# Optimization experiments

Hardware: AMD Instinct MI355X
Metric: run time of the kernel (lower is better)

Reference implementation:

```python
import jax, jax.numpy as jnp
import numpy as np

RADIUS = 2.0  # ball-query radius (float forward arg in the original; fixed here)


def _conv1x1(x, W, b):
    # 1x1 Conv2D over NHWC == per-point linear layer
    return jnp.einsum('bmsc,cd->bmsd', x, W) + b


def _ball_query(xyz, new_xyz, radius, nsample):
    """For each cluster center, take the first (by index) nsample points within
    radius, padding with the first found neighbor (TF ball-query semantics).
    xyz: (B,N,3), new_xyz: (B,M,3) -> idx (B,M,nsample) int32."""
    N = xyz.shape[1]
    d2 = jnp.sum((new_xyz[:, :, None, :] - xyz[:, None, :, :]) ** 2, axis=-1)  # (B,M,N)
    valid = d2 < radius * radius
    key = jnp.where(valid, jnp.arange(N, dtype=jnp.int32)[None, None, :], N)
    order = jnp.argsort(key, axis=-1)[..., :nsample]          # (B,M,nsample)
    skey = jnp.take_along_axis(key, order, axis=-1)
    idx = jnp.where(skey < N, order, order[..., :1])          # pad with first neighbor
    return idx


def setup_inputs() -> dict:
    key = jax.random.key(0)
    ks = jax.random.split(key, 8)
    B, N = 8, 8192
    xyz = jax.random.normal(ks[0], (B, N, 3), dtype=jnp.float32)

    def w(k, cin, cout):
        return (jax.random.normal(k, (cin, cout), dtype=jnp.float32) / np.sqrt(cin)).astype(jnp.float32)

    z = lambda c: jnp.zeros((c,), jnp.float32)
    inp = {
        'xyz': xyz,
        'W1': w(ks[1], 3, 64),    'b1': z(64),
        'W2': w(ks[2], 64, 128),  'b2': z(128),
        'W3': w(ks[3], 128, 256), 'b3': z(256),
        'W4': w(ks[4], 256, 128), 'b4': z(128),
        'W5': w(ks[5], 128, 64),  'b5': z(64),
        'Wa': w(ks[6], 64, 1),    'ba': z(1),
        'Wo': w(ks[7], 64, 2),    'bo': z(2),
        'num_clusters': 512,
        'num_samples': 64,
    }
    return inp


def reference(xyz, W1, b1, W2, b2, W3, b3, W4, b4, W5, b5, Wa, ba, Wo, bo,
              num_clusters, num_samples):
    # sample cluster centers (deterministic stand-in for random subsampling)
    new_xyz = xyz[:, :num_clusters]                                    # (B,M,3)
    idx = _ball_query(xyz, new_xyz, RADIUS, num_samples)               # (B,M,S)
    grouped = jax.vmap(lambda pts, i: pts[i])(xyz, idx)                # (B,M,S,3)
    g = (grouped - new_xyz[:, :, None, :]) / RADIUS                    # normalize_radius

    # shared per-point MLP (1x1 convs, relu)
    h = jax.nn.relu(_conv1x1(g, W1, b1))
    h = jax.nn.relu(_conv1x1(h, W2, b2))
    h = jax.nn.relu(_conv1x1(h, W3, b3))
    # MaxPoolAxis: max over samples, keepdims
    h = jnp.max(h, axis=2, keepdims=True)                              # (B,M,1,256)
    # mlp2 convs (linear, no activation in source)
    h = _conv1x1(h, W4, b4)
    h = _conv1x1(h, W5, b5)                                            # (B,M,1,64)

    attention = jax.nn.softplus(_conv1x1(h, Wa, ba))[:, :, 0, 0]       # (B,M)
    o = _conv1x1(h, Wo, bo)[:, :, 0, :]                                # (B,M,2)
    o = o / jnp.sqrt(jnp.maximum(jnp.sum(o * o, axis=-1, keepdims=True), 1e-8))
    orientation = jnp.arctan2(o[..., 1], o[..., 0])                    # (B,M)
    return new_xyz, idx, attention, orientation
```

## Files before the change

kernel.cpp:

```cpp
#include <hip/hip_runtime.h>
#include <math.h>

#define BB 8
#define NN 8192
#define MM 512
#define SS 64
#define NCLUST (BB*MM)

#define OUT_IDX   (BB*MM*3)
#define OUT_ATT   (OUT_IDX + BB*MM*SS)
#define OUT_ORI   (OUT_ATT + BB*MM)

#define WS_W3 8192
#define WS_V  40960

typedef short v8s __attribute__((ext_vector_type(8)));
typedef float v4f __attribute__((ext_vector_type(4)));

static __device__ __forceinline__ unsigned short f2bf(float x) {
    unsigned int u = __float_as_uint(x);
    u += 0x7FFFu + ((u >> 16) & 1u);
    return (unsigned short)(u >> 16);
}

__global__ void pack_weights(const float* __restrict__ W2,
                             const float* __restrict__ W3,
                             unsigned short* __restrict__ ws)
{
    const int gid = blockIdx.x * 256 + threadIdx.x;
    const float* W; unsigned short* dst; int N, kt, nt, lane;
    if (gid < 1024) {
        W = W2; N = 128;
        const int tile = gid >> 6; lane = gid & 63;
        kt = tile >> 3; nt = tile & 7;
        dst = ws + (size_t)(tile * 64 + lane) * 8;
    } else {
        const int g = gid - 1024;
        W = W3; N = 256;
        const int tile = g >> 6; lane = g & 63;
        kt = tile >> 4; nt = tile & 15;
        dst = ws + WS_W3 + (size_t)(tile * 64 + lane) * 8;
    }
    const int k0 = kt * 32 + (lane >> 4) * 8;
    const int n  = nt * 16 + (lane & 15);
    union { unsigned short u[8]; v8s v; } f;
    #pragma unroll
    for (int j = 0; j < 8; ++j) f.u[j] = f2bf(W[(k0 + j) * N + n]);
    *(v8s*)dst = f.v;
}

__global__ __launch_bounds__(256, 4) void feat3d_front(
    const float* __restrict__ xyz,
    const float* __restrict__ W1, const float* __restrict__ b1,
    const float* __restrict__ b2, const float* __restrict__ b3,
    const unsigned short* __restrict__ Wp,
    unsigned short* __restrict__ vdst,
    float* __restrict__ out)
{
    __shared__ __align__(16) unsigned char lds[27200];
    unsigned short* a2p = (unsigned short*)lds;
    unsigned short* a3p = (unsigned short*)(lds + 8192);
    float* smallf       = (float*)(lds + 24576);
    int* ls_idx         = (int*)(lds + 26624);
    unsigned long long* ls_mask = (unsigned long long*)(lds + 26880);

    float* ls_g  = smallf;
    float* ls_w1 = smallf + 256;

    const int t   = threadIdx.x;
    const int wv  = t >> 6;
    const int l   = t & 63;
    const int q   = l >> 4;
    const int r16 = l & 15;
    const int blk = blockIdx.x;
    const int b   = blk >> 9;
    const int m   = blk & 511;
    const float* xb = xyz + (size_t)b * (NN * 3);

    const v8s* W2f = (const v8s*)Wp;
    v8s bfr[2][2];
    #pragma unroll
    for (int kt = 0; kt < 2; ++kt)
        #pragma unroll
        for (int ni = 0; ni < 2; ++ni)
            bfr[kt][ni] = W2f[(kt*8 + 2*wv + ni)*64 + l];

    const float cx = xb[m*3+0], cy = xb[m*3+1], cz = xb[m*3+2];

    if (t < 3) out[(b*MM + m)*3 + t] = xb[m*3 + t];

    if (t < 64) {
        ls_w1[t*4+0] = W1[t];
        ls_w1[t*4+1] = W1[64 + t];
        ls_w1[t*4+2] = W1[128 + t];
        ls_w1[t*4+3] = b1[t];
    }

    int cnt = 0;
    {
        int base = 0, pb = 0;
        while (base < NN && cnt < SS) {
            const int j = base + t;
            const float dx = xb[j*3+0] - cx;
            const float dy = xb[j*3+1] - cy;
            const float dz = xb[j*3+2] - cz;
            const float d2 = __fadd_rn(__fadd_rn(__fmul_rn(dx,dx), __fmul_rn(dy,dy)),
                                       __fmul_rn(dz,dz));
            const bool valid = d2 < 4.0f;
            const unsigned long long mask = __ballot(valid);
            if (l == 0) ls_mask[pb*4 + wv] = mask;
            __syncthreads();
            const unsigned long long m0 = ls_mask[pb*4+0], m1 = ls_mask[pb*4+1],
                                     m2 = ls_mask[pb*4+2], m3 = ls_mask[pb*4+3];
            int below = __popcll(mask & ((1ull << l) - 1ull));
            if (wv > 0) below += (int)__popcll(m0);
            if (wv > 1) below += (int)__popcll(m1);
            if (wv > 2) below += (int)__popcll(m2);
            const int pos = cnt + below;
            if (valid && pos < SS) {
                ls_idx[pos]   = j;
                ls_g[pos*4+0] = dx * 0.5f;
                ls_g[pos*4+1] = dy * 0.5f;
                ls_g[pos*4+2] = dz * 0.5f;
            }
            cnt += (int)(__popcll(m0) + __popcll(m1) + __popcll(m2) + __popcll(m3));
            if (cnt > SS) cnt = SS;
            base += 256;
            pb ^= 1;
        }
    }
    __syncthreads();
    if (t < SS && t >= cnt) {
        ls_idx[t]   = ls_idx[0];
        ls_g[t*4+0] = ls_g[0];
        ls_g[t*4+1] = ls_g[1];
        ls_g[t*4+2] = ls_g[2];
    }
    __syncthreads();
    if (t < 64) out[OUT_IDX + (b*MM + m)*SS + t] = (float)ls_idx[t];

    {
        const int s = wv*16 + r16;
        const float4 g4 = *(const float4*)&ls_g[s*4];
        #pragma unroll
        for (int kt = 0; kt < 2; ++kt) {
            union { unsigned short u[8]; v8s v; } fr;
            #pragma unroll
            for (int j = 0; j < 8; ++j) {
                const int c = kt*32 + q*8 + j;
                const float4 w = *(const float4*)&ls_w1[c*4];
                const float h = fmaf(g4.x, w.x, fmaf(g4.y, w.y, fmaf(g4.z, w.z, w.w)));
                fr.u[j] = f2bf(fmaxf(h, 0.f));
            }
            *(v8s*)&a2p[((kt*4 + wv)*64 + l)*8] = fr.v;
        }
    }
    __syncthreads();

    {
        const v4f z = {0.f, 0.f, 0.f, 0.f};
        v4f acc[4][2];
        #pragma unroll
        for (int mt = 0; mt < 4; ++mt) { acc[mt][0] = z; acc[mt][1] = z; }

        #pragma unroll
        for (int kt = 0; kt < 2; ++kt)
            #pragma unroll
            for (int mt = 0; mt < 4; ++mt) {
                const v8s a = *(const v8s*)&a2p[((kt*4 + mt)*64 + l)*8];
                #pragma unroll
                for (int ni = 0; ni < 2; ++ni)
                    acc[mt][ni] = __builtin_amdgcn_mfma_f32_16x16x32_bf16(
                        a, bfr[kt][ni], acc[mt][ni], 0, 0, 0);
            }

        #pragma unroll
        for (int ni = 0; ni < 2; ++ni) {
            const int c2  = (2*wv + ni)*16 + r16;
            const float bias = b2[c2];
            const int kt3 = c2 >> 5;
            const int lhi = ((c2 >> 3) & 3) << 4;
            const int j3  = c2 & 7;
            #pragma unroll
            for (int mt = 0; mt < 4; ++mt)
                #pragma unroll
                for (int rg = 0; rg < 4; ++rg) {
                    const float h = fmaxf(acc[mt][ni][rg] + bias, 0.f);
                    const int s15 = q*4 + rg;
                    a3p[((kt3*4 + mt)*64 + (lhi | s15))*8 + j3] = f2bf(h);
                }
        }
    }
    __syncthreads();

    {
        const v8s* W3f = (const v8s*)(Wp + WS_W3);
        const int cg = blk;
        unsigned short* vrow = vdst + (size_t)cg * 256;

        #pragma unroll
        for (int np = 0; np < 2; ++np) {
            const int nt0 = 4*wv + 2*np;
            const v4f z = {0.f, 0.f, 0.f, 0.f};
            v4f acc[4][2];
            #pragma unroll
            for (int mt = 0; mt < 4; ++mt) { acc[mt][0] = z; acc[mt][1] = z; }

            v8s bb0 = W3f[(0*16 + nt0    )*64 + l];
            v8s bb1 = W3f[(0*16 + nt0 + 1)*64 + l];
            #pragma unroll
            for (int kt = 0; kt < 4; ++kt) {
                v8s a[4];
                #pragma unroll
                for (int mt = 0; mt < 4; ++mt)
                    a[mt] = *(const v8s*)&a3p[((kt*4 + mt)*64 + l)*8];
                v8s nb0, nb1;
                if (kt < 3) {
                    nb0 = W3f[((kt+1)*16 + nt0    )*64 + l];
                    nb1 = W3f[((kt+1)*16 + nt0 + 1)*64 + l];
                }
                #pragma unroll
                for (int mt = 0; mt < 4; ++mt) {
                    acc[mt][0] = __builtin_amdgcn_mfma_f32_16x16x32_bf16(
                        a[mt], bb0, acc[mt][0], 0, 0, 0);
                    acc[mt][1] = __builtin_amdgcn_mfma_f32_16x16x32_bf16(
                        a[mt], bb1, acc[mt][1], 0, 0, 0);
                }
                if (kt < 3) { bb0 = nb0; bb1 = nb1; }
            }

            #pragma unroll
            for (int ni = 0; ni < 2; ++ni) {
                float mx = acc[0][ni][0];
                #pragma unroll
                for (int mt = 0; mt < 4; ++mt)
                    #pragma unroll
                    for (int rg = 0; rg < 4; ++rg)
                        mx = fmaxf(mx, acc[mt][ni][rg]);
                mx = fmaxf(mx, __shfl_xor(mx, 16));
                mx = fmaxf(mx, __shfl_xor(mx, 32));
                if (q == 0) {
                    const int c = (nt0 + ni)*16 + r16;
                    vrow[c] = f2bf(fmaxf(mx + b3[c], 0.f));
                }
            }
        }
    }
}

__global__ __launch_bounds__(256) void feat3d_tail(
    const unsigned short* __restrict__ vsrc,
    const float* __restrict__ W4, const float* __restrict__ b4,
    const float* __restrict__ W5, const float* __restrict__ b5,
    const float* __restrict__ Wa, const float* __restrict__ ba,
    const float* __restrict__ Wo, const float* __restrict__ bo,
    float* __restrict__ out)
{
    __shared__ __align__(16) float V[16][256];
    __shared__ __align__(16) float H4[16][128];
    __shared__ __align__(16) float H5[16][64];

    const int t   = threadIdx.x;
    const int cl0 = blockIdx.x * 16;

    {
        const int i  = t >> 4;
        const int ch = t & 15;
        const uint4* src = (const uint4*)(vsrc + (size_t)(cl0 + i) * 256);
        #pragma unroll
        for (int h = 0; h < 2; ++h) {
            const uint4 r = src[ch*2 + h];
            const unsigned int u[4] = {r.x, r.y, r.z, r.w};
            #pragma unroll
            for (int j = 0; j < 4; ++j) {
                V[i][ch*16 + h*8 + 2*j]     = __uint_as_float(u[j] << 16);
                V[i][ch*16 + h*8 + 2*j + 1] = __uint_as_float(u[j] & 0xFFFF0000u);
            }
        }
    }
    __syncthreads();

    {
        const int c  = t & 127;
        const int ih = t >> 7;
        float acc[8];
        #pragma unroll
        for (int i = 0; i < 8; ++i) acc[i] = b4[c];
        for (int k4 = 0; k4 < 64; ++k4) {
            const float w0 = W4[(4*k4+0)*128 + c];
            const float w1 = W4[(4*k4+1)*128 + c];
            const float w2 = W4[(4*k4+2)*128 + c];
            const float w3 = W4[(4*k4+3)*128 + c];
            #pragma unroll
            for (int i = 0; i < 8; ++i) {
                const float4 vv = *(const float4*)&V[ih*8 + i][4*k4];
                acc[i] = fmaf(vv.x, w0, fmaf(vv.y, w1,
                         fmaf(vv.z, w2, fmaf(vv.w, w3, acc[i]))));
            }
        }
        #pragma unroll
        for (int i = 0; i < 8; ++i) H4[ih*8 + i][c] = acc[i];
    }
    __syncthreads();

    {
        const int c  = t & 63;
        const int iq = t >> 6;
        float acc[4];
        #pragma unroll
        for (int i = 0; i < 4; ++i) acc[i] = b5[c];
        for (int k4 = 0; k4 < 32; ++k4) {
            const float w0 = W5[(4*k4+0)*64 + c];
            const float w1 = W5[(4*k4+1)*64 + c];
            const float w2 = W5[(4*k4+2)*64 + c];
            const float w3 = W5[(4*k4+3)*64 + c];
            #pragma unroll
            for (int i = 0; i < 4; ++i) {
                const float4 vv = *(const float4*)&H4[iq*4 + i][4*k4];
                acc[i] = fmaf(vv.x, w0, fmaf(vv.y, w1,
                         fmaf(vv.z, w2, fmaf(vv.w, w3, acc[i]))));
            }
        }
        #pragma unroll
        for (int i = 0; i < 4; ++i) H5[iq*4 + i][c] = acc[i];
    }
    __syncthreads();

    {
        const int wv = t >> 6, l = t & 63;
        const float wa  = Wa[l];
        const float wo0 = Wo[2*l + 0];
        const float wo1 = Wo[2*l + 1];
        #pragma unroll
        for (int i = 0; i < 4; ++i) {
            const float hv = H5[4*wv + i][l];
            float va = hv * wa;
            float v0 = hv * wo0;
            float v1 = hv * wo1;
            #pragma unroll
            for (int off = 32; off > 0; off >>= 1) {
                va += __shfl_down(va, off);
                v0 += __shfl_down(v0, off);
                v1 += __shfl_down(v1, off);
            }
            if (l == 0) {
                const int cg = cl0 + 4*wv + i;
                const float a = va + ba[0];
                out[OUT_ATT + cg] = fmaxf(a, 0.f) + log1pf(expf(-fabsf(a)));
                out[OUT_ORI + cg] = atan2f(v1 + bo[1], v0 + bo[0]);
            }
        }
    }
}

extern "C" void kernel_launch(void* const* d_in, const int* in_sizes, int n_in,
                              void* d_out, int out_size, void* d_ws, size_t ws_size,
                              hipStream_t stream) {
    const float* xyz = (const float*)d_in[0];
    const float* W1  = (const float*)d_in[1];
    const float* b1  = (const float*)d_in[2];
    const float* W2  = (const float*)d_in[3];
    const float* b2  = (const float*)d_in[4];
    const float* W3  = (const float*)d_in[5];
    const float* b3  = (const float*)d_in[6];
    const float* W4  = (const float*)d_in[7];
    const float* b4  = (const float*)d_in[8];
    const float* W5  = (const float*)d_in[9];
    const float* b5  = (const float*)d_in[10];
    const float* Wa  = (const float*)d_in[11];
    const float* ba  = (const float*)d_in[12];
    const float* Wo  = (const float*)d_in[13];
    const float* bo  = (const float*)d_in[14];

    unsigned short* ws = (unsigned short*)d_ws;

    pack_weights<<<dim3(20), dim3(256), 0, stream>>>(W2, W3, ws);
    feat3d_front<<<dim3(NCLUST), dim3(256), 0, stream>>>(
        xyz, W1, b1, b2, b3, ws, ws + WS_V, (float*)d_out);
    feat3d_tail<<<dim3(NCLUST/16), dim3(256), 0, stream>>>(
        ws + WS_V, W4, b4, W5, b5, Wa, ba, Wo, bo, (float*)d_out);
}
```

Baseline: 139.0 us.

## Process two clusters per block with per-wave ball query and shared MLP tiles

Each block now handles two cluster centers, with waves 0 and 1 each doing an independent wave-local ball query using ballot prefix counts, removing the block-wide barrier in every scan iteration. The MLP MFMA stages are widened to 128 rows so W2/W3 fragments loaded per wave are reused across both clusters, halving weight traffic per cluster and the block count. In exchange, LDS use grows, register pressure rises (occupancy bound lowered to 3), half the waves idle during the query, and each query scans only 64 points per step.

```diff
diff --git a/kernel.cpp b/kernel.cpp
--- a/kernel.cpp
+++ b/kernel.cpp
@@ -49,7 +49,7 @@
     *(v8s*)dst = f.v;
 }
 
-__global__ __launch_bounds__(256, 4) void feat3d_front(
+__global__ __launch_bounds__(256, 3) void feat3d_front(
     const float* __restrict__ xyz,
     const float* __restrict__ W1, const float* __restrict__ b1,
     const float* __restrict__ b2, const float* __restrict__ b3,
@@ -57,24 +57,20 @@
     unsigned short* __restrict__ vdst,
     float* __restrict__ out)
 {
-    __shared__ __align__(16) unsigned char lds[27200];
+    __shared__ __align__(16) unsigned char lds[52736];
     unsigned short* a2p = (unsigned short*)lds;
-    unsigned short* a3p = (unsigned short*)(lds + 8192);
-    float* smallf       = (float*)(lds + 24576);
-    int* ls_idx         = (int*)(lds + 26624);
-    unsigned long long* ls_mask = (unsigned long long*)(lds + 26880);
-
-    float* ls_g  = smallf;
-    float* ls_w1 = smallf + 256;
+    unsigned short* a3p = (unsigned short*)(lds + 16384);
+    float* ls_g  = (float*)(lds + 49152);
+    float* ls_w1 = (float*)(lds + 51200);
+    int*   ls_idx= (int*)(lds + 52224);
 
     const int t   = threadIdx.x;
     const int wv  = t >> 6;
     const int l   = t & 63;
     const int q   = l >> 4;
     const int r16 = l & 15;
-    const int blk = blockIdx.x;
-    const int b   = blk >> 9;
-    const int m   = blk & 511;
+    const int cg0 = blockIdx.x * 2;
+    const int b   = cg0 >> 9;
     const float* xb = xyz + (size_t)b * (NN * 3);
 
     const v8s* W2f = (const v8s*)Wp;
@@ -85,22 +81,24 @@
         for (int ni = 0; ni < 2; ++ni)
             bfr[kt][ni] = W2f[(kt*8 + 2*wv + ni)*64 + l];
 
-    const float cx = xb[m*3+0], cy = xb[m*3+1], cz = xb[m*3+2];
-
-    if (t < 3) out[(b*MM + m)*3 + t] = xb[m*3 + t];
-
-    if (t < 64) {
-        ls_w1[t*4+0] = W1[t];
-        ls_w1[t*4+1] = W1[64 + t];
-        ls_w1[t*4+2] = W1[128 + t];
-        ls_w1[t*4+3] = b1[t];
-    }
-
-    int cnt = 0;
-    {
-        int base = 0, pb = 0;
+    if (t >= 128 && t < 192) {
+        const int tt = t - 128;
+        ls_w1[tt*4+0] = W1[tt];
+        ls_w1[tt*4+1] = W1[64 + tt];
+        ls_w1[tt*4+2] = W1[128 + tt];
+        ls_w1[tt*4+3] = b1[tt];
+    }
+
+    if (wv < 2) {
+        const int cg = cg0 + wv;
+        const int m  = cg & 511;
+        const float cx = xb[m*3+0], cy = xb[m*3+1], cz = xb[m*3+2];
+        if (l < 3) out[cg*3 + l] = xb[m*3 + l];
+        float* gdst = ls_g  + wv * 256;
+        int*   idst = ls_idx + wv * 64;
+        int cnt = 0, base = 0;
         while (base < NN && cnt < SS) {
-            const int j = base + t;
+            const int j = base + l;
             const float dx = xb[j*3+0] - cx;
             const float dy = xb[j*3+1] - cy;
             const float dz = xb[j*3+2] - cz;
@@ -108,70 +106,66 @@
                                        __fmul_rn(dz,dz));
             const bool valid = d2 < 4.0f;
             const unsigned long long mask = __ballot(valid);
-            if (l == 0) ls_mask[pb*4 + wv] = mask;
-            __syncthreads();
-            const unsigned long long m0 = ls_mask[pb*4+0], m1 = ls_mask[pb*4+1],
-                                     m2 = ls_mask[pb*4+2], m3 = ls_mask[pb*4+3];
-            int below = __popcll(mask & ((1ull << l) - 1ull));
-            if (wv > 0) below += (int)__popcll(m0);
-            if (wv > 1) below += (int)__popcll(m1);
-            if (wv > 2) below += (int)__popcll(m2);
+            const int below = __popcll(mask & ((1ull << l) - 1ull));
             const int pos = cnt + below;
             if (valid && pos < SS) {
-                ls_idx[pos]   = j;
-                ls_g[pos*4+0] = dx * 0.5f;
-                ls_g[pos*4+1] = dy * 0.5f;
-                ls_g[pos*4+2] = dz * 0.5f;
-            }
-            cnt += (int)(__popcll(m0) + __popcll(m1) + __popcll(m2) + __popcll(m3));
+                idst[pos]   = j;
+                gdst[pos*4+0] = dx * 0.5f;
+                gdst[pos*4+1] = dy * 0.5f;
+                gdst[pos*4+2] = dz * 0.5f;
+            }
+            cnt += (int)__popcll(mask);
             if (cnt > SS) cnt = SS;
-            base += 256;
-            pb ^= 1;
-        }
-    }
-    __syncthreads();
-    if (t < SS && t >= cnt) {
-        ls_idx[t]   = ls_idx[0];
-        ls_g[t*4+0] = ls_g[0];
-        ls_g[t*4+1] = ls_g[1];
-        ls_g[t*4+2] = ls_g[2];
-    }
-    __syncthreads();
-    if (t < 64) out[OUT_IDX + (b*MM + m)*SS + t] = (float)ls_idx[t];
-
-    {
-        const int s = wv*16 + r16;
-        const float4 g4 = *(const float4*)&ls_g[s*4];
-        #pragma unroll
-        for (int kt = 0; kt < 2; ++kt) {
-            union { unsigned short u[8]; v8s v; } fr;
-            #pragma unroll
-            for (int j = 0; j < 8; ++j) {
-                const int c = kt*32 + q*8 + j;
-                const float4 w = *(const float4*)&ls_w1[c*4];
-                const float h = fmaf(g4.x, w.x, fmaf(g4.y, w.y, fmaf(g4.z, w.z, w.w)));
-                fr.u[j] = f2bf(fmaxf(h, 0.f));
-            }
-            *(v8s*)&a2p[((kt*4 + wv)*64 + l)*8] = fr.v;
+            base += 64;
+        }
+        if (l >= cnt) {
+            idst[l]     = idst[0];
+            gdst[l*4+0] = gdst[0];
+            gdst[l*4+1] = gdst[1];
+            gdst[l*4+2] = gdst[2];
+        }
+        out[OUT_IDX + cg*SS + l] = (float)idst[l];
+    }
+    __syncthreads();
+
+    {
+        #pragma unroll
+        for (int cc = 0; cc < 2; ++cc) {
+            const int rr = cc*64 + wv*16 + r16;
+            const int mt = rr >> 4;
+            const float4 g4 = *(const float4*)&ls_g[rr*4];
+            #pragma unroll
+            for (int kt = 0; kt < 2; ++kt) {
+                union { unsigned short u[8]; v8s v; } fr;
+                #pragma unroll
+                for (int j = 0; j < 8; ++j) {
+                    const int c = kt*32 + q*8 + j;
+                    const float4 w = *(const float4*)&ls_w1[c*4];
+                    const float h = fmaf(g4.x, w.x, fmaf(g4.y, w.y,
+                                    fmaf(g4.z, w.z, w.w)));
+                    fr.u[j] = f2bf(fmaxf(h, 0.f));
+                }
+                *(v8s*)&a2p[((kt*8 + mt)*64 + l)*8] = fr.v;
+            }
         }
     }
     __syncthreads();
 
     {
         const v4f z = {0.f, 0.f, 0.f, 0.f};
-        v4f acc[4][2];
-        #pragma unroll
-        for (int mt = 0; mt < 4; ++mt) { acc[mt][0] = z; acc[mt][1] = z; }
+        v4f acc[8][2];
+        #pragma unroll
+        for (int mt = 0; mt < 8; ++mt) { acc[mt][0] = z; acc[mt][1] = z; }
 
         #pragma unroll
         for (int kt = 0; kt < 2; ++kt)
             #pragma unroll
-            for (int mt = 0; mt < 4; ++mt) {
-                const v8s a = *(const v8s*)&a2p[((kt*4 + mt)*64 + l)*8];
-                #pragma unroll
-                for (int ni = 0; ni < 2; ++ni)
-                    acc[mt][ni] = __builtin_amdgcn_mfma_f32_16x16x32_bf16(
-                        a, bfr[kt][ni], acc[mt][ni], 0, 0, 0);
+            for (int mt = 0; mt < 8; ++mt) {
+                const v8s a = *(const v8s*)&a2p[((kt*8 + mt)*64 + l)*8];
+                acc[mt][0] = __builtin_amdgcn_mfma_f32_16x16x32_bf16(
+                    a, bfr[kt][0], acc[mt][0], 0, 0, 0);
+                acc[mt][1] = __builtin_amdgcn_mfma_f32_16x16x32_bf16(
+                    a, bfr[kt][1], acc[mt][1], 0, 0, 0);
             }
 
         #pragma unroll
@@ -182,12 +176,12 @@
             const int lhi = ((c2 >> 3) & 3) << 4;
             const int j3  = c2 & 7;
             #pragma unroll
-            for (int mt = 0; mt < 4; ++mt)
+            for (int mt = 0; mt < 8; ++mt)
                 #pragma unroll
                 for (int rg = 0; rg < 4; ++rg) {
                     const float h = fmaxf(acc[mt][ni][rg] + bias, 0.f);
                     const int s15 = q*4 + rg;
-                    a3p[((kt3*4 + mt)*64 + (lhi | s15))*8 + j3] = f2bf(h);
+                    a3p[((kt3*8 + mt)*64 + (lhi | s15))*8 + j3] = f2bf(h);
                 }
         }
     }
@@ -195,32 +189,32 @@
 
     {
         const v8s* W3f = (const v8s*)(Wp + WS_W3);
-        const int cg = blk;
-        unsigned short* vrow = vdst + (size_t)cg * 256;
+        unsigned short* vrow0 = vdst + (size_t)cg0 * 256;
+        unsigned short* vrow1 = vdst + (size_t)(cg0 + 1) * 256;
 
         #pragma unroll
         for (int np = 0; np < 2; ++np) {
             const int nt0 = 4*wv + 2*np;
             const v4f z = {0.f, 0.f, 0.f, 0.f};
-            v4f acc[4][2];
-            #pragma unroll
-            for (int mt = 0; mt < 4; ++mt) { acc[mt][0] = z; acc[mt][1] = z; }
-
-            v8s bb0 = W3f[(0*16 + nt0    )*64 + l];
-            v8s bb1 = W3f[(0*16 + nt0 + 1)*64 + l];
+            v4f acc[8][2];
+            #pragma unroll
+            for (int mt = 0; mt < 8; ++mt) { acc[mt][0] = z; acc[mt][1] = z; }
+
+            v8s bb0 = W3f[(nt0    )*64 + l];
+            v8s bb1 = W3f[(nt0 + 1)*64 + l];
             #pragma unroll
             for (int kt = 0; kt < 4; ++kt) {
-                v8s a[4];
-                #pragma unroll
-                for (int mt = 0; mt < 4; ++mt)
-                    a[mt] = *(const v8s*)&a3p[((kt*4 + mt)*64 + l)*8];
+                v8s a[8];
+                #pragma unroll
+                for (int mt = 0; mt < 8; ++mt)
+                    a[mt] = *(const v8s*)&a3p[((kt*8 + mt)*64 + l)*8];
                 v8s nb0, nb1;
                 if (kt < 3) {
                     nb0 = W3f[((kt+1)*16 + nt0    )*64 + l];
                     nb1 = W3f[((kt+1)*16 + nt0 + 1)*64 + l];
                 }
                 #pragma unroll
-                for (int mt = 0; mt < 4; ++mt) {
+                for (int mt = 0; mt < 8; ++mt) {
                     acc[mt][0] = __builtin_amdgcn_mfma_f32_16x16x32_bf16(
                         a[mt], bb0, acc[mt][0], 0, 0, 0);
                     acc[mt][1] = __builtin_amdgcn_mfma_f32_16x16x32_bf16(
@@ -231,17 +225,23 @@
 
             #pragma unroll
             for (int ni = 0; ni < 2; ++ni) {
-                float mx = acc[0][ni][0];
+                float mx0 = acc[0][ni][0], mx1 = acc[4][ni][0];
                 #pragma unroll
                 for (int mt = 0; mt < 4; ++mt)
                     #pragma unroll
-                    for (int rg = 0; rg < 4; ++rg)
-                        mx = fmaxf(mx, acc[mt][ni][rg]);
-                mx = fmaxf(mx, __shfl_xor(mx, 16));
-                mx = fmaxf(mx, __shfl_xor(mx, 32));
+                    for (int rg = 0; rg < 4; ++rg) {
+                        mx0 = fmaxf(mx0, acc[mt    ][ni][rg]);
+                        mx1 = fmaxf(mx1, acc[mt + 4][ni][rg]);
+                    }
+                mx0 = fmaxf(mx0, __shfl_xor(mx0, 16));
+                mx0 = fmaxf(mx0, __shfl_xor(mx0, 32));
+                mx1 = fmaxf(mx1, __shfl_xor(mx1, 16));
+                mx1 = fmaxf(mx1, __shfl_xor(mx1, 32));
                 if (q == 0) {
                     const int c = (nt0 + ni)*16 + r16;
-                    vrow[c] = f2bf(fmaxf(mx + b3[c], 0.f));
+                    const float bc = b3[c];
+                    vrow0[c] = f2bf(fmaxf(mx0 + bc, 0.f));
+                    vrow1[c] = f2bf(fmaxf(mx1 + bc, 0.f));
                 }
             }
         }
@@ -375,7 +375,7 @@
     unsigned short* ws = (unsigned short*)d_ws;
 
     pack_weights<<<dim3(20), dim3(256), 0, stream>>>(W2, W3, ws);
-    feat3d_front<<<dim3(NCLUST), dim3(256), 0, stream>>>(
+    feat3d_front<<<dim3(NCLUST/2), dim3(256), 0, stream>>>(
         xyz, W1, b1, b2, b3, ws, ws + WS_V, (float*)d_out);
     feat3d_tail<<<dim3(NCLUST/16), dim3(256), 0, stream>>>(
         ws + WS_V, W4, b4, W5, b5, Wa, ba, Wo, bo, (float*)d_out);
```

Result: slower. 156.0 us (+12.3%).

## Split ball query into its own wave-per-cluster kernel before the MLP kernel

Applied to the files above, without the earlier changes.

Moves the ball query out of the fused front kernel into a separate kernel where each 64-lane wave handles one cluster, so the scan needs only a wave ballot instead of block-wide LDS mask exchange and __syncthreads every iteration. Grouped offsets go to a global workspace that the MLP kernel then reads, which now has smaller LDS and a higher occupancy hint. In exchange it adds a kernel launch and a global round trip for the grouped coordinates, and each wave scans 64 points per step instead of 256 per block.

```diff
diff --git a/kernel.cpp b/kernel.cpp
--- a/kernel.cpp
+++ b/kernel.cpp
@@ -13,6 +13,7 @@
 
 #define WS_W3 8192
 #define WS_V  40960
+#define WS_G  1089536
 
 typedef short v8s __attribute__((ext_vector_type(8)));
 typedef float v4f __attribute__((ext_vector_type(4)));
@@ -49,23 +50,67 @@
     *(v8s*)dst = f.v;
 }
 
-__global__ __launch_bounds__(256, 4) void feat3d_front(
+__global__ __launch_bounds__(256, 8) void feat3d_bq(
     const float* __restrict__ xyz,
+    float* __restrict__ gws,
+    float* __restrict__ out)
+{
+    const int t  = threadIdx.x;
+    const int l  = t & 63;
+    const int cg = blockIdx.x * 4 + (t >> 6);
+    const int b  = cg >> 9;
+    const int m  = cg & 511;
+    const float* xb = xyz + (size_t)b * (NN * 3);
+
+    const float cx = xb[m*3+0], cy = xb[m*3+1], cz = xb[m*3+2];
+    if (l < 3) out[cg*3 + l] = xb[m*3 + l];
+
+    float4* gdst = (float4*)(gws + (size_t)cg * 256);
+    float*  idst = out + OUT_IDX + (size_t)cg * SS;
+
+    int cnt = 0, base = 0, fIdx = -1;
+    float fx = 0.f, fy = 0.f, fz = 0.f;
+    while (base < NN && cnt < SS) {
+        const int j = base + l;
+        const float dx = xb[j*3+0] - cx;
+        const float dy = xb[j*3+1] - cy;
+        const float dz = xb[j*3+2] - cz;
+        const float d2 = __fadd_rn(__fadd_rn(__fmul_rn(dx,dx), __fmul_rn(dy,dy)),
+                                   __fmul_rn(dz,dz));
+        const bool valid = d2 < 4.0f;
+        const unsigned long long mask = __ballot(valid);
+        const int below = __popcll(mask & ((1ull << l) - 1ull));
+        const int pos = cnt + below;
+        if (valid && pos < SS) {
+            gdst[pos] = make_float4(dx*0.5f, dy*0.5f, dz*0.5f, 0.f);
+            idst[pos] = (float)j;
+        }
+        if (fIdx < 0 && mask != 0ull) {
+            const int fl = (int)__builtin_ctzll(mask);
+            fIdx = base + fl;
+            fx = __shfl(dx, fl); fy = __shfl(dy, fl); fz = __shfl(dz, fl);
+        }
+        cnt += (int)__popcll(mask);
+        if (cnt > SS) cnt = SS;
+        base += 64;
+    }
+    if (l >= cnt) {
+        gdst[l] = make_float4(fx*0.5f, fy*0.5f, fz*0.5f, 0.f);
+        idst[l] = (float)fIdx;
+    }
+}
+
+__global__ __launch_bounds__(256, 5) void feat3d_mlp(
+    const float* __restrict__ gws,
     const float* __restrict__ W1, const float* __restrict__ b1,
     const float* __restrict__ b2, const float* __restrict__ b3,
     const unsigned short* __restrict__ Wp,
-    unsigned short* __restrict__ vdst,
-    float* __restrict__ out)
+    unsigned short* __restrict__ vdst)
 {
-    __shared__ __align__(16) unsigned char lds[27200];
+    __shared__ __align__(16) unsigned char lds[25600];
     unsigned short* a2p = (unsigned short*)lds;
     unsigned short* a3p = (unsigned short*)(lds + 8192);
-    float* smallf       = (float*)(lds + 24576);
-    int* ls_idx         = (int*)(lds + 26624);
-    unsigned long long* ls_mask = (unsigned long long*)(lds + 26880);
-
-    float* ls_g  = smallf;
-    float* ls_w1 = smallf + 256;
+    float* ls_w1        = (float*)(lds + 24576);
 
     const int t   = threadIdx.x;
     const int wv  = t >> 6;
@@ -73,9 +118,6 @@
     const int q   = l >> 4;
     const int r16 = l & 15;
     const int blk = blockIdx.x;
-    const int b   = blk >> 9;
-    const int m   = blk & 511;
-    const float* xb = xyz + (size_t)b * (NN * 3);
 
     const v8s* W2f = (const v8s*)Wp;
     v8s bfr[2][2];
@@ -85,9 +127,8 @@
         for (int ni = 0; ni < 2; ++ni)
             bfr[kt][ni] = W2f[(kt*8 + 2*wv + ni)*64 + l];
 
-    const float cx = xb[m*3+0], cy = xb[m*3+1], cz = xb[m*3+2];
-
-    if (t < 3) out[(b*MM + m)*3 + t] = xb[m*3 + t];
+    const int s = wv*16 + r16;
+    const float4 g4 = *(const float4*)(gws + (size_t)blk*256 + s*4);
 
     if (t < 64) {
         ls_w1[t*4+0] = W1[t];
@@ -95,53 +136,9 @@
         ls_w1[t*4+2] = W1[128 + t];
         ls_w1[t*4+3] = b1[t];
     }
-
-    int cnt = 0;
-    {
-        int base = 0, pb = 0;
-        while (base < NN && cnt < SS) {
-            const int j = base + t;
-            const float dx = xb[j*3+0] - cx;
-            const float dy = xb[j*3+1] - cy;
-            const float dz = xb[j*3+2] - cz;
-            const float d2 = __fadd_rn(__fadd_rn(__fmul_rn(dx,dx), __fmul_rn(dy,dy)),
-                                       __fmul_rn(dz,dz));
-            const bool valid = d2 < 4.0f;
-            const unsigned long long mask = __ballot(valid);
-            if (l == 0) ls_mask[pb*4 + wv] = mask;
-            __syncthreads();
-            const unsigned long long m0 = ls_mask[pb*4+0], m1 = ls_mask[pb*4+1],
-                                     m2 = ls_mask[pb*4+2], m3 = ls_mask[pb*4+3];
-            int below = __popcll(mask & ((1ull << l) - 1ull));
-            if (wv > 0) below += (int)__popcll(m0);
-            if (wv > 1) below += (int)__popcll(m1);
-            if (wv > 2) below += (int)__popcll(m2);
-            const int pos = cnt + below;
-            if (valid && pos < SS) {
-                ls_idx[pos]   = j;
-                ls_g[pos*4+0] = dx * 0.5f;
-                ls_g[pos*4+1] = dy * 0.5f;
-                ls_g[pos*4+2] = dz * 0.5f;
-            }
-            cnt += (int)(__popcll(m0) + __popcll(m1) + __popcll(m2) + __popcll(m3));
-            if (cnt > SS) cnt = SS;
-            base += 256;
-            pb ^= 1;
-        }
-    }
-    __syncthreads();
-    if (t < SS && t >= cnt) {
-        ls_idx[t]   = ls_idx[0];
-        ls_g[t*4+0] = ls_g[0];
-        ls_g[t*4+1] = ls_g[1];
-        ls_g[t*4+2] = ls_g[2];
-    }
-    __syncthreads();
-    if (t < 64) out[OUT_IDX + (b*MM + m)*SS + t] = (float)ls_idx[t];
-
-    {
-        const int s = wv*16 + r16;
-        const float4 g4 = *(const float4*)&ls_g[s*4];
+    __syncthreads();
+
+    {
         #pragma unroll
         for (int kt = 0; kt < 2; ++kt) {
             union { unsigned short u[8]; v8s v; } fr;
@@ -149,7 +146,8 @@
             for (int j = 0; j < 8; ++j) {
                 const int c = kt*32 + q*8 + j;
                 const float4 w = *(const float4*)&ls_w1[c*4];
-                const float h = fmaf(g4.x, w.x, fmaf(g4.y, w.y, fmaf(g4.z, w.z, w.w)));
+                const float h = fmaf(g4.x, w.x, fmaf(g4.y, w.y,
+                                fmaf(g4.z, w.z, w.w)));
                 fr.u[j] = f2bf(fmaxf(h, 0.f));
             }
             *(v8s*)&a2p[((kt*4 + wv)*64 + l)*8] = fr.v;
@@ -168,10 +166,10 @@
             #pragma unroll
             for (int mt = 0; mt < 4; ++mt) {
                 const v8s a = *(const v8s*)&a2p[((kt*4 + mt)*64 + l)*8];
-                #pragma unroll
-                for (int ni = 0; ni < 2; ++ni)
-                    acc[mt][ni] = __builtin_amdgcn_mfma_f32_16x16x32_bf16(
-                        a, bfr[kt][ni], acc[mt][ni], 0, 0, 0);
+                acc[mt][0] = __builtin_amdgcn_mfma_f32_16x16x32_bf16(
+                    a, bfr[kt][0], acc[mt][0], 0, 0, 0);
+                acc[mt][1] = __builtin_amdgcn_mfma_f32_16x16x32_bf16(
+                    a, bfr[kt][1], acc[mt][1], 0, 0, 0);
             }
 
         #pragma unroll
@@ -195,8 +193,7 @@
 
     {
         const v8s* W3f = (const v8s*)(Wp + WS_W3);
-        const int cg = blk;
-        unsigned short* vrow = vdst + (size_t)cg * 256;
+        unsigned short* vrow = vdst + (size_t)blk * 256;
 
         #pragma unroll
         for (int np = 0; np < 2; ++np) {
@@ -206,8 +203,8 @@
             #pragma unroll
             for (int mt = 0; mt < 4; ++mt) { acc[mt][0] = z; acc[mt][1] = z; }
 
-            v8s bb0 = W3f[(0*16 + nt0    )*64 + l];
-            v8s bb1 = W3f[(0*16 + nt0 + 1)*64 + l];
+            v8s bb0 = W3f[(nt0    )*64 + l];
+            v8s bb1 = W3f[(nt0 + 1)*64 + l];
             #pragma unroll
             for (int kt = 0; kt < 4; ++kt) {
                 v8s a[4];
@@ -373,10 +370,13 @@
     const float* bo  = (const float*)d_in[14];
 
     unsigned short* ws = (unsigned short*)d_ws;
+    float* gws = (float*)(ws + WS_G);
 
     pack_weights<<<dim3(20), dim3(256), 0, stream>>>(W2, W3, ws);
-    feat3d_front<<<dim3(NCLUST), dim3(256), 0, stream>>>(
-        xyz, W1, b1, b2, b3, ws, ws + WS_V, (float*)d_out);
+    feat3d_bq<<<dim3(NCLUST/4), dim3(256), 0, stream>>>(
+        xyz, gws, (float*)d_out);
+    feat3d_mlp<<<dim3(NCLUST), dim3(256), 0, stream>>>(
+        gws, W1, b1, b2, b3, ws, ws + WS_V);
     feat3d_tail<<<dim3(NCLUST/16), dim3(256), 0, stream>>>(
         ws + WS_V, W4, b4, W5, b5, Wa, ba, Wo, bo, (float*)d_out);
 }
```

New measurement: 192.5 us. 1.39x slower.
